# Optimization experiments

Measured on AMD Instinct MI355X. Metric: run time of the kernel, lower is better.

Reference implementation:

```python
import jax, jax.numpy as jnp
import numpy as np

# Module dims (match init_kwargs): c_in=1, khop=3, f=128, c_out=2, f_out=128
N, KHOP, NNB, C_IN, F_IN = 2048, 3, 16, 1, 128
C_OUT, F_OUT = 2, 128
EPS_ROOT, EPS_NORM = 1e-8, 1e-7


def setup_inputs() -> dict:
    key = jax.random.key(0)
    k1, k2, k3 = jax.random.split(key, 3)
    x = jax.random.normal(k1, (N, C_IN, F_IN), jnp.float32)
    # dense form of the ragged neighbor[i][k] -> (n, c, f) lists
    neighbor = jax.random.normal(k2, (N, KHOP, NNB, C_IN, F_IN), jnp.float32)
    # Conv1d(khop*c_in, c_out*f_out, kernel_size=f, bias=False) weight
    W = jax.random.normal(k3, (C_OUT * F_OUT, KHOP * C_IN, F_IN), jnp.float32) * 0.05
    return {"x": x, "neighbor": neighbor, "W": W}


def _sgnroot(a):
    return jnp.sign(a) * jnp.sqrt(jnp.clip(jnp.abs(a), EPS_ROOT))


def _row_normalize(a):
    a = a / (jnp.abs(a).sum(-2, keepdims=True) + EPS_NORM)
    return jnp.where(jnp.isnan(a), 0.0, a)


def _feature_adjacency(x, neighbor):
    # x: (N,c,f), neighbor: (N,k,n,c,f) -> fadj: (N,k,f,f)
    fadj = jnp.einsum('Nca,Nkncb->Nkab', x, neighbor)
    fadj = fadj + jnp.swapaxes(fadj, -1, -2)
    return _row_normalize(_sgnroot(fadj))


def _transform(z, adj, W):
    # z: (..., c, f); adj: (..., K, f, f) broadcastable against z's batch dims
    # y[..., K, c, a] = sum_b adj[..., K, a, b] * z[..., c, b]
    y = jnp.einsum('...kab,...cb->...kca', adj, z)
    y = y.reshape(y.shape[:-3] + (KHOP * C_IN, F_IN))  # (..., k*c, f)
    # Conv1d with kernel_size == f and output length 1 == full contraction
    out = jnp.einsum('oqf,...qf->...o', W, y)
    return out.reshape(out.shape[:-1] + (C_OUT, F_OUT))


def reference(x, neighbor, W):
    adj = _feature_adjacency(x, neighbor)                     # (N,k,f,f)
    x_out = _transform(x, adj, W)                             # (N,c_out,f_out)
    # each neighbor[i,k] is transformed with the full per-sample adj[i]
    nbr_out = _transform(neighbor, adj[:, None, None], W)     # (N,k,n,c_out,f_out)
    return (x_out, nbr_out)
```

## Files before the change

kernel.cpp:

```cpp
#include <hip/hip_runtime.h>

typedef unsigned short u16;
typedef unsigned int u32;
typedef __bf16 bf16;
typedef __bf16 bf16x8 __attribute__((ext_vector_type(8)));
typedef __bf16 bf16x4 __attribute__((ext_vector_type(4)));
typedef float f32x4 __attribute__((ext_vector_type(4)));

#define NSAMP 2048
#define KH 3
#define NNBR 16
#define F 128
#define OUT_O 256
#define QT 384

#define ZLD 136
#define YLD 136

__device__ __forceinline__ bf16x4 cvt4(float4 v) {
    bf16x4 h;
    h[0] = (bf16)v.x; h[1] = (bf16)v.y; h[2] = (bf16)v.z; h[3] = (bf16)v.w;
    return h;
}

__global__ void wprep(const float* __restrict__ W, bf16* __restrict__ Wbf) {
    int i = blockIdx.x * 256 + threadIdx.x;
    if (i < OUT_O * QT) Wbf[i] = (bf16)W[i];
}

__launch_bounds__(512, 4)
__global__ void featkhop(const float* __restrict__ xg,
                         const float* __restrict__ ng,
                         const bf16* __restrict__ Wbf,
                         float* __restrict__ out) {
    __shared__ __align__(16) bf16 Zs[64 * ZLD];
    __shared__ __align__(16) bf16 Ys[2][64 * YLD];
    float* const xls = (float*)(Zs + 49 * ZLD);
    float* const sls = xls + F;
    float* const rsi = xls + 4 * F;

    const int i = blockIdx.x;
    const int t = threadIdx.x;
    const int lane = t & 63;
    const int w = t >> 6;
    const int lr = lane & 15;
    const int lg = lane >> 4;

    if (t < F / 4) {
        float4 v = *(const float4*)(xg + (size_t)i * F + t * 4);
        *(float4*)(xls + t * 4) = v;
        *(bf16x4*)(Zs + 0 * ZLD + t * 4) = cvt4(v);
    }
    {
        const float* nb = ng + (size_t)i * (KH * NNBR * F);
        #pragma unroll
        for (int c = 0; c < 3; ++c) {
            int j = c * 512 + t;
            float4 v = *(const float4*)(nb + j * 4);
            int fl = j * 4;
            int row = 1 + (fl >> 7);
            int b = fl & 127;
            *(bf16x4*)(Zs + row * ZLD + b) = cvt4(v);
        }
    }
    __syncthreads();

    if (t < KH * F) {
        int q = t >> 7, b = t & 127;
        float s = 0.f;
        #pragma unroll
        for (int n = 0; n < NNBR; ++n) s += (float)Zs[(1 + q * NNBR + n) * ZLD + b];
        sls[q * F + b] = s;
    }
    __syncthreads();

    const int a_row = w * 16 + lr;
    const float x_a = xls[a_row];
    const int cbase = lg * 8;

    f32x4 acc2[4][2];
    {
        f32x4 zf = {0.f, 0.f, 0.f, 0.f};
        #pragma unroll
        for (int mt = 0; mt < 4; ++mt) { acc2[mt][0] = zf; acc2[mt][1] = zf; }
    }

    for (int q = 0; q < KH; ++q) {
        const float s_a = sls[q * F + a_row];
        float uv[32];
        float ps = 0.f;
        #pragma unroll
        for (int kk = 0; kk < 4; ++kk) {
            float4 xb0 = *(const float4*)(xls + kk * 32 + cbase);
            float4 xb1 = *(const float4*)(xls + kk * 32 + cbase + 4);
            float4 sb0 = *(const float4*)(sls + q * F + kk * 32 + cbase);
            float4 sb1 = *(const float4*)(sls + q * F + kk * 32 + cbase + 4);
            float xb[8] = {xb0.x, xb0.y, xb0.z, xb0.w, xb1.x, xb1.y, xb1.z, xb1.w};
            float sb[8] = {sb0.x, sb0.y, sb0.z, sb0.w, sb1.x, sb1.y, sb1.z, sb1.w};
            #pragma unroll
            for (int e = 0; e < 8; ++e) {
                float tv = x_a * sb[e] + xb[e] * s_a;
                float r = tv * __builtin_amdgcn_rsqf(fmaxf(fabsf(tv), 1e-8f));
                uv[kk * 8 + e] = r;
                ps += fabsf(r);
            }
        }
        ps += __shfl_xor(ps, 16);
        ps += __shfl_xor(ps, 32);
        if (lg == 0) rsi[a_row] = __builtin_amdgcn_rcpf(ps + 1e-7f);
        __syncthreads();

        bf16* Ysb = Ys[q & 1];
        f32x4 acc1[4];
        {
            f32x4 zf = {0.f, 0.f, 0.f, 0.f};
            #pragma unroll
            for (int mt = 0; mt < 4; ++mt) acc1[mt] = zf;
        }
        #pragma unroll
        for (int kk = 0; kk < 4; ++kk) {
            float4 r0 = *(const float4*)(rsi + kk * 32 + cbase);
            float4 r1 = *(const float4*)(rsi + kk * 32 + cbase + 4);
            float rb[8] = {r0.x, r0.y, r0.z, r0.w, r1.x, r1.y, r1.z, r1.w};
            bf16x8 afrag;
            #pragma unroll
            for (int e = 0; e < 8; ++e)
                afrag[e] = (bf16)(uv[kk * 8 + e] * rb[e]);
            #pragma unroll
            for (int mt = 0; mt < 4; ++mt) {
                bf16x8 zfrag = *(const bf16x8*)(Zs + (mt * 16 + lr) * ZLD + kk * 32 + cbase);
                acc1[mt] = __builtin_amdgcn_mfma_f32_16x16x32_bf16(afrag, zfrag, acc1[mt], 0, 0, 0);
            }
        }
        #pragma unroll
        for (int mt = 0; mt < 4; ++mt) {
            bf16x4 yv;
            #pragma unroll
            for (int r = 0; r < 4; ++r) yv[r] = (bf16)acc1[mt][r];
            *(bf16x4*)(Ysb + (mt * 16 + lr) * YLD + w * 16 + lg * 4) = yv;
        }
        __syncthreads();

        #pragma unroll
        for (int kk = 0; kk < 4; ++kk) {
            const bf16* wp = Wbf + (size_t)(w * 32 + lr) * QT + q * F + kk * 32 + cbase;
            bf16x8 bf0 = *(const bf16x8*)wp;
            bf16x8 bf1 = *(const bf16x8*)(wp + 16 * QT);
            #pragma unroll
            for (int mt = 0; mt < 4; ++mt) {
                bf16x8 af = *(const bf16x8*)(Ysb + (mt * 16 + lr) * YLD + kk * 32 + cbase);
                acc2[mt][0] = __builtin_amdgcn_mfma_f32_16x16x32_bf16(af, bf0, acc2[mt][0], 0, 0, 0);
                acc2[mt][1] = __builtin_amdgcn_mfma_f32_16x16x32_bf16(af, bf1, acc2[mt][1], 0, 0, 0);
            }
        }
    }

    float* xout = out + (size_t)i * OUT_O;
    float* nout = out + (size_t)NSAMP * OUT_O + (size_t)i * 48 * OUT_O;
    #pragma unroll
    for (int mt = 0; mt < 4; ++mt) {
        #pragma unroll
        for (int r = 0; r < 4; ++r) {
            int v = mt * 16 + lg * 4 + r;
            #pragma unroll
            for (int nn = 0; nn < 2; ++nn) {
                int o = w * 32 + nn * 16 + lr;
                float val = acc2[mt][nn][r];
                if (v == 0) xout[o] = val;
                else if (v <= 48) nout[(size_t)(v - 1) * OUT_O + o] = val;
            }
        }
    }
}

extern "C" void kernel_launch(void* const* d_in, const int* in_sizes, int n_in,
                              void* d_out, int out_size, void* d_ws, size_t ws_size,
                              hipStream_t stream) {
    const float* x   = (const float*)d_in[0];
    const float* nbr = (const float*)d_in[1];
    const float* W   = (const float*)d_in[2];
    bf16* Wbf = (bf16*)d_ws;
    wprep<<<(OUT_O * QT + 255) / 256, 256, 0, stream>>>(W, Wbf);
    featkhop<<<NSAMP, 512, 0, stream>>>(x, nbr, Wbf, (float*)d_out);
}
```

Baseline: 82.09 us.

## Cut register pressure for higher occupancy and drop the post-load barrier

Raises the launch-bounds occupancy hint from 4 to 6 blocks per CU. To help fit that budget, intermediate sqrt values are stored as packed bf16 instead of fp32, and the first MFMA loop is reordered so only one accumulator is live at a time. The neighbor-sum now reads fp32 data directly from global memory instead of the bf16 copy in LDS, which removes a __syncthreads but re-reads global memory (likely cache hits) and makes the sums more precise. Rounding the sqrt values to bf16 before normalization adds one extra rounding step.

```diff
diff --git a/kernel.cpp b/kernel.cpp
--- a/kernel.cpp
+++ b/kernel.cpp
@@ -28,7 +28,7 @@
     if (i < OUT_O * QT) Wbf[i] = (bf16)W[i];
 }
 
-__launch_bounds__(512, 4)
+__launch_bounds__(512, 6)
 __global__ void featkhop(const float* __restrict__ xg,
                          const float* __restrict__ ng,
                          const bf16* __restrict__ Wbf,
@@ -51,8 +51,8 @@
         *(float4*)(xls + t * 4) = v;
         *(bf16x4*)(Zs + 0 * ZLD + t * 4) = cvt4(v);
     }
+    const float* nb = ng + (size_t)i * (KH * NNBR * F);
     {
-        const float* nb = ng + (size_t)i * (KH * NNBR * F);
         #pragma unroll
         for (int c = 0; c < 3; ++c) {
             int j = c * 512 + t;
@@ -63,13 +63,11 @@
             *(bf16x4*)(Zs + row * ZLD + b) = cvt4(v);
         }
     }
-    __syncthreads();
-
     if (t < KH * F) {
         int q = t >> 7, b = t & 127;
         float s = 0.f;
         #pragma unroll
-        for (int n = 0; n < NNBR; ++n) s += (float)Zs[(1 + q * NNBR + n) * ZLD + b];
+        for (int n = 0; n < NNBR; ++n) s += nb[(q * NNBR + n) * F + b];
         sls[q * F + b] = s;
     }
     __syncthreads();
@@ -87,7 +85,7 @@
 
     for (int q = 0; q < KH; ++q) {
         const float s_a = sls[q * F + a_row];
-        float uv[32];
+        bf16x8 uvh[4];
         float ps = 0.f;
         #pragma unroll
         for (int kk = 0; kk < 4; ++kk) {
@@ -101,7 +99,7 @@
             for (int e = 0; e < 8; ++e) {
                 float tv = x_a * sb[e] + xb[e] * s_a;
                 float r = tv * __builtin_amdgcn_rsqf(fmaxf(fabsf(tv), 1e-8f));
-                uv[kk * 8 + e] = r;
+                uvh[kk][e] = (bf16)r;
                 ps += fabsf(r);
             }
         }
@@ -110,33 +108,29 @@
         if (lg == 0) rsi[a_row] = __builtin_amdgcn_rcpf(ps + 1e-7f);
         __syncthreads();
 
-        bf16* Ysb = Ys[q & 1];
-        f32x4 acc1[4];
-        {
-            f32x4 zf = {0.f, 0.f, 0.f, 0.f};
-            #pragma unroll
-            for (int mt = 0; mt < 4; ++mt) acc1[mt] = zf;
-        }
+        bf16x8 afrag[4];
         #pragma unroll
         for (int kk = 0; kk < 4; ++kk) {
             float4 r0 = *(const float4*)(rsi + kk * 32 + cbase);
             float4 r1 = *(const float4*)(rsi + kk * 32 + cbase + 4);
             float rb[8] = {r0.x, r0.y, r0.z, r0.w, r1.x, r1.y, r1.z, r1.w};
-            bf16x8 afrag;
             #pragma unroll
             for (int e = 0; e < 8; ++e)
-                afrag[e] = (bf16)(uv[kk * 8 + e] * rb[e]);
-            #pragma unroll
-            for (int mt = 0; mt < 4; ++mt) {
-                bf16x8 zfrag = *(const bf16x8*)(Zs + (mt * 16 + lr) * ZLD + kk * 32 + cbase);
-                acc1[mt] = __builtin_amdgcn_mfma_f32_16x16x32_bf16(afrag, zfrag, acc1[mt], 0, 0, 0);
-            }
+                afrag[kk][e] = (bf16)((float)uvh[kk][e] * rb[e]);
         }
+
+        bf16* Ysb = Ys[q & 1];
         #pragma unroll
         for (int mt = 0; mt < 4; ++mt) {
+            f32x4 a1 = {0.f, 0.f, 0.f, 0.f};
+            #pragma unroll
+            for (int kk = 0; kk < 4; ++kk) {
+                bf16x8 zfrag = *(const bf16x8*)(Zs + (mt * 16 + lr) * ZLD + kk * 32 + cbase);
+                a1 = __builtin_amdgcn_mfma_f32_16x16x32_bf16(afrag[kk], zfrag, a1, 0, 0, 0);
+            }
             bf16x4 yv;
             #pragma unroll
-            for (int r = 0; r < 4; ++r) yv[r] = (bf16)acc1[mt][r];
+            for (int r = 0; r < 4; ++r) yv[r] = (bf16)a1[r];
             *(bf16x4*)(Ysb + (mt * 16 + lr) * YLD + w * 16 + lg * 4) = yv;
         }
         __syncthreads();
@@ -144,13 +138,13 @@
         #pragma unroll
         for (int kk = 0; kk < 4; ++kk) {
             const bf16* wp = Wbf + (size_t)(w * 32 + lr) * QT + q * F + kk * 32 + cbase;
-            bf16x8 bf0 = *(const bf16x8*)wp;
-            bf16x8 bf1 = *(const bf16x8*)(wp + 16 * QT);
+            bf16x8 wf0 = *(const bf16x8*)wp;
+            bf16x8 wf1 = *(const bf16x8*)(wp + 16 * QT);
             #pragma unroll
             for (int mt = 0; mt < 4; ++mt) {
                 bf16x8 af = *(const bf16x8*)(Ysb + (mt * 16 + lr) * YLD + kk * 32 + cbase);
-                acc2[mt][0] = __builtin_amdgcn_mfma_f32_16x16x32_bf16(af, bf0, acc2[mt][0], 0, 0, 0);
-                acc2[mt][1] = __builtin_amdgcn_mfma_f32_16x16x32_bf16(af, bf1, acc2[mt][1], 0, 0, 0);
+                acc2[mt][0] = __builtin_amdgcn_mfma_f32_16x16x32_bf16(af, wf0, acc2[mt][0], 0, 0, 0);
+                acc2[mt][1] = __builtin_amdgcn_mfma_f32_16x16x32_bf16(af, wf1, acc2[mt][1], 0, 0, 0);
             }
         }
     }
```

Measured after the change: 95.85 us. 16.8% more time.
